# Kernel optimization log

Measured on AMD Instinct MI355X. Metric: run time of the kernel, lower is better.

The kernel has to match this reference:

```python
import jax, jax.numpy as jnp
import numpy as np

QUERY_DIM = 192
KEY_DIM = 64
DIM_OUT = 128
C = QUERY_DIM + KEY_DIM  # 256
N = 10000
E = 320000
M = 5000


def setup_inputs() -> dict:
    key = jax.random.key(0)
    ks = jax.random.split(key, 16)
    s = 1.0 / np.sqrt(C)
    inp = {
        "query": jax.random.normal(ks[0], (N, QUERY_DIM), jnp.float32),
        "key_idx": jax.random.randint(ks[1], (N,), 0, KEY_DIM),
        "edge_index": jax.random.randint(ks[2], (2, E), 0, N),
        "mask_idx": jnp.sort(jax.random.randint(ks[3], (M,), 0, N)),
        "Wq": jax.random.normal(ks[4], (C, C), jnp.float32) * s,
        "bq": jnp.zeros((C,), jnp.float32),
        "Wk": jax.random.normal(ks[5], (C, C), jnp.float32) * s,
        "bk": jnp.zeros((C,), jnp.float32),
        "Wv": jax.random.normal(ks[6], (C, C), jnp.float32) * s,
        "bv": jnp.zeros((C,), jnp.float32),
        "Ws": jax.random.normal(ks[7], (C, C), jnp.float32) * s,
        "bs": jnp.zeros((C,), jnp.float32),
        "Wo": jax.random.normal(ks[8], (KEY_DIM, DIM_OUT), jnp.float32) * (1.0 / np.sqrt(KEY_DIM)),
        "bo": jnp.zeros((DIM_OUT,), jnp.float32),
    }
    return inp


def reference(query, key_idx, edge_index, mask_idx, Wq, bq, Wk, bk, Wv, bv, Ws, bs, Wo, bo):
    # node features: [N, C] = concat(query, one_hot(key))
    x = jnp.concatenate([query, jax.nn.one_hot(key_idx, KEY_DIM, dtype=query.dtype)], axis=1)
    src, dst = edge_index[0], edge_index[1]  # messages flow src -> dst
    # node-level projections (dense GEMMs), then edge gather
    q_n = x @ Wq + bq
    k_n = x @ Wk + bk
    v_n = x @ Wv + bv
    q = q_n[dst]  # [E, C]
    k = k_n[src]
    v = v_n[src]
    score = jnp.sum(q * k, axis=-1) / jnp.sqrt(jnp.asarray(C, x.dtype))  # [E]
    # per-destination softmax over incoming edges
    m = jax.ops.segment_max(score, dst, num_segments=N)  # [N]
    m = jnp.where(jnp.isfinite(m), m, 0.0)
    e = jnp.exp(score - m[dst])
    denom = jax.ops.segment_sum(e, dst, num_segments=N)
    alpha = e / (denom[dst] + 1e-16)
    # scatter-aggregate weighted values + root/skip connection
    agg = jax.ops.segment_sum(alpha[:, None] * v, dst, num_segments=N)  # [N, C]
    out = agg + (x @ Ws + bs)
    h = jax.nn.relu(out[mask_idx])  # [M, C]
    h = h[:, QUERY_DIM:]  # [M, KEY_DIM]
    return h @ Wo + bo  # [M, DIM_OUT]
```

## Files before the change

### kernel.cpp

```cpp
#include <hip/hip_runtime.h>

#define QDIM 192
#define KDIM 64
#define CDIM 256
#define DOUT 128
#define CAP 128
#define NEG_INF __int_as_float(0xFF800000)
#define LDP 200

typedef _Float16 hf2 __attribute__((ext_vector_type(2)));
typedef _Float16 half4 __attribute__((ext_vector_type(4)));
typedef _Float16 half8 __attribute__((ext_vector_type(8)));
typedef float floatx4 __attribute__((ext_vector_type(4)));

#if defined(__has_builtin)
#if __has_builtin(__builtin_amdgcn_fdot2)
#define HAVE_FDOT2 1
#endif
#endif

__device__ __forceinline__ hf2 bc_h2(unsigned u) { return __builtin_bit_cast(hf2, u); }

__device__ __forceinline__ float dot2acc(hf2 a, hf2 b, float c) {
#ifdef HAVE_FDOT2
    return __builtin_amdgcn_fdot2(a, b, c, false);
#else
    return c + (float)a[0] * (float)b[0] + (float)a[1] * (float)b[1];
#endif
}

__global__ __launch_bounds__(256) void gemm_scatter(
        const float* __restrict__ query, const int* __restrict__ key_idx,
        const float* Wq, const float* bq, const float* Wk, const float* bk,
        const float* Wv, const float* bv, const float* Ws, const float* bs,
        const int* __restrict__ esrc, const int* __restrict__ edst,
        int* __restrict__ deg, int* __restrict__ adj, int E,
        _Float16* __restrict__ Qbuf, _Float16* __restrict__ Kbuf,
        _Float16* __restrict__ Vbuf, float* __restrict__ Sbuf, int N) {
    __shared__ __align__(16) _Float16 As[64 * LDP];
    __shared__ __align__(16) _Float16 Bs[64 * LDP];
    int bm = blockIdx.x * 64;
    int tid = threadIdx.x;

    {
        int total = gridDim.x * gridDim.y * 256;
        int gid = (blockIdx.y * gridDim.x + blockIdx.x) * 256 + tid;
        for (int e = gid; e < E; e += total) {
            int d = edst[e];
            int slot = atomicAdd(&deg[d], 1);
            if (slot < CAP) adj[d * CAP + slot] = esrc[e];
        }
    }

    #pragma unroll
    for (int it = 0; it < 12; it++) {
        int idx = tid + it * 256;
        int r = idx / 48, f4 = idx % 48;
        int gr = bm + r;
        float4 va = make_float4(0.f, 0.f, 0.f, 0.f);
        if (gr < N) va = ((const float4*)(query + (size_t)gr * QDIM))[f4];
        half4 h = { (_Float16)va.x, (_Float16)va.y, (_Float16)va.z, (_Float16)va.w };
        *((half4*)&As[r * LDP + f4 * 4]) = h;
    }

    int w = tid >> 6, l = tid & 63;
    int lrow = l & 15, quad = l >> 4;

    int ki[4];
    #pragma unroll
    for (int reg = 0; reg < 4; reg++) {
        int gr = bm + w * 16 + quad * 4 + reg;
        ki[reg] = (gr < N) ? key_idx[gr] : 0;
    }

    for (int t = 0; t < 2; t++) {
        int bn = blockIdx.y * 128 + t * 64;
        const float* Wb; const float* bvec; int wc0;
        if (bn < 256)      { Wb = Wq; bvec = bq; wc0 = bn; }
        else if (bn < 512) { Wb = Wk; bvec = bk; wc0 = bn - 256; }
        else if (bn < 576) { Wb = Wv; bvec = bv; wc0 = QDIM + (bn - 512); }
        else               { Wb = Ws; bvec = bs; wc0 = QDIM + (bn - 576); }

        if (t > 0) __syncthreads();
        {
            int c = tid & 63, r0 = tid >> 6;
            #pragma unroll
            for (int it = 0; it < 6; it++) {
                int kg = r0 + it * 4;
                float f[8];
                #pragma unroll
                for (int j = 0; j < 8; j++)
                    f[j] = Wb[(size_t)(kg * 8 + j) * CDIM + wc0 + c];
                half8 h8 = { (_Float16)f[0], (_Float16)f[1], (_Float16)f[2], (_Float16)f[3],
                             (_Float16)f[4], (_Float16)f[5], (_Float16)f[6], (_Float16)f[7] };
                *((half8*)&Bs[c * LDP + kg * 8]) = h8;
            }
        }
        __syncthreads();

        floatx4 acc[4] = {{0.f,0.f,0.f,0.f},{0.f,0.f,0.f,0.f},{0.f,0.f,0.f,0.f},{0.f,0.f,0.f,0.f}};
        const _Float16* arow = &As[(w * 16 + lrow) * LDP + quad * 8];
        #pragma unroll
        for (int ks = 0; ks < 6; ks++) {
            half8 af = *(const half8*)(arow + ks * 32);
            #pragma unroll
            for (int nt = 0; nt < 4; nt++) {
                half8 bf = *(const half8*)(&Bs[(nt * 16 + lrow) * LDP + quad * 8 + ks * 32]);
                acc[nt] = __builtin_amdgcn_mfma_f32_16x16x32_f16(af, bf, acc[nt], 0, 0, 0);
            }
        }

        #pragma unroll
        for (int nt = 0; nt < 4; nt++) {
            int gc = bn + nt * 16 + lrow;
            int wc = wc0 + nt * 16 + lrow;
            float bias = bvec[wc];
            #pragma unroll
            for (int reg = 0; reg < 4; reg++) {
                int gr = bm + w * 16 + quad * 4 + reg;
                if (gr < N) {
                    float v = acc[nt][reg] + Wb[(size_t)(QDIM + ki[reg]) * CDIM + wc] + bias;
                    if (gc < 256)      Qbuf[(size_t)gr * 256 + gc] = (_Float16)v;
                    else if (gc < 512) Kbuf[(size_t)gr * 256 + (gc - 256)] = (_Float16)v;
                    else if (gc < 576) Vbuf[(size_t)gr * KDIM + (gc - 512)] = (_Float16)v;
                    else               Sbuf[(size_t)gr * KDIM + (gc - 576)] = v;
                }
            }
        }
    }
}

__global__ __launch_bounds__(256) void attend_out(
        const _Float16* __restrict__ Qbuf, const _Float16* __restrict__ Kbuf,
        const _Float16* __restrict__ Vbuf, const float* __restrict__ Sbuf,
        const int* __restrict__ deg, const int* __restrict__ adj,
        const int* __restrict__ mask, const float* __restrict__ Wo,
        const float* __restrict__ bo, float* __restrict__ out, int M) {
    int w = threadIdx.x >> 6, lane = threadIdx.x & 63;
    int r = blockIdx.x * 4 + w;
    if (r >= M) return;
    int node = mask[r];
    if (r > 0 && mask[r - 1] == node) return;
    int l = lane & 15, g = lane >> 4;

    const uint4* qp = (const uint4*)(Qbuf + (size_t)node * 256 + l * 16);
    uint4 qa = qp[0], qb = qp[1];
    hf2 qh[8] = { bc_h2(qa.x), bc_h2(qa.y), bc_h2(qa.z), bc_h2(qa.w),
                  bc_h2(qb.x), bc_h2(qb.y), bc_h2(qb.z), bc_h2(qb.w) };

    int dn = min(deg[node], CAP);
    const int* arow = adj + (size_t)node * CAP;

    float m = NEG_INF, dsum = 0.f;
    float a0 = 0.f, a1 = 0.f, a2 = 0.f, a3 = 0.f;
    for (int i = g; i < dn; i += 4) {
        int s = arow[i];
        const uint4* kp = (const uint4*)(Kbuf + (size_t)s * 256 + l * 16);
        uint4 ka = kp[0], kb = kp[1];
        float d = 0.f;
        d = dot2acc(bc_h2(ka.x), qh[0], d);
        d = dot2acc(bc_h2(ka.y), qh[1], d);
        d = dot2acc(bc_h2(ka.z), qh[2], d);
        d = dot2acc(bc_h2(ka.w), qh[3], d);
        d = dot2acc(bc_h2(kb.x), qh[4], d);
        d = dot2acc(bc_h2(kb.y), qh[5], d);
        d = dot2acc(bc_h2(kb.z), qh[6], d);
        d = dot2acc(bc_h2(kb.w), qh[7], d);
        d += __shfl_xor(d, 1, 64);
        d += __shfl_xor(d, 2, 64);
        d += __shfl_xor(d, 4, 64);
        d += __shfl_xor(d, 8, 64);
        float sc = d * 0.0625f;
        float m_new = fmaxf(m, sc);
        float scale = __expf(m - m_new);
        float p = __expf(sc - m_new);
        dsum = dsum * scale + p;
        uint2 vv = *(const uint2*)(Vbuf + (size_t)s * KDIM + l * 4);
        hf2 v01 = bc_h2(vv.x), v23 = bc_h2(vv.y);
        a0 = a0 * scale + p * (float)v01[0];
        a1 = a1 * scale + p * (float)v01[1];
        a2 = a2 * scale + p * (float)v23[0];
        a3 = a3 * scale + p * (float)v23[1];
        m = m_new;
    }

    float Mx = fmaxf(m, __shfl_xor(m, 16, 64));
    Mx = fmaxf(Mx, __shfl_xor(Mx, 32, 64));
    float wgt = (m == NEG_INF) ? 0.f : __expf(m - Mx);
    float ds = dsum * wgt;
    ds += __shfl_xor(ds, 16, 64);
    ds += __shfl_xor(ds, 32, 64);
    a0 *= wgt; a1 *= wgt; a2 *= wgt; a3 *= wgt;
    a0 += __shfl_xor(a0, 16, 64); a0 += __shfl_xor(a0, 32, 64);
    a1 += __shfl_xor(a1, 16, 64); a1 += __shfl_xor(a1, 32, 64);
    a2 += __shfl_xor(a2, 16, 64); a2 += __shfl_xor(a2, 32, 64);
    a3 += __shfl_xor(a3, 16, 64); a3 += __shfl_xor(a3, 32, 64);
    float inv = 1.f / (ds + 1e-16f);

    float4 s4 = *((const float4*)(Sbuf + (size_t)node * KDIM + l * 4));
    float h0 = fmaxf(a0 * inv + s4.x, 0.f);
    float h1 = fmaxf(a1 * inv + s4.y, 0.f);
    float h2 = fmaxf(a2 * inv + s4.z, 0.f);
    float h3 = fmaxf(a3 * inv + s4.w, 0.f);

    float o0 = bo[lane], o1 = bo[lane + 64];
    #pragma unroll
    for (int c = 0; c < KDIM; c++) {
        float hc = (c & 3) == 0 ? h0 : (c & 3) == 1 ? h1 : (c & 3) == 2 ? h2 : h3;
        float hv = __shfl(hc, c >> 2, 64);
        o0 += hv * Wo[c * DOUT + lane];
        o1 += hv * Wo[c * DOUT + 64 + lane];
    }
    int rr = r;
    do {
        out[(size_t)rr * DOUT + lane] = o0;
        out[(size_t)rr * DOUT + 64 + lane] = o1;
        rr++;
    } while (rr < M && mask[rr] == node);
}

extern "C" void kernel_launch(void* const* d_in, const int* in_sizes, int n_in,
                              void* d_out, int out_size, void* d_ws, size_t ws_size,
                              hipStream_t stream) {
    const float* query    = (const float*)d_in[0];
    const int* key_idx    = (const int*)d_in[1];
    const int* edge_index = (const int*)d_in[2];
    const int* mask_idx   = (const int*)d_in[3];
    const float* Wq = (const float*)d_in[4];
    const float* bq = (const float*)d_in[5];
    const float* Wk = (const float*)d_in[6];
    const float* bk = (const float*)d_in[7];
    const float* Wv = (const float*)d_in[8];
    const float* bv = (const float*)d_in[9];
    const float* Ws = (const float*)d_in[10];
    const float* bs = (const float*)d_in[11];
    const float* Wo = (const float*)d_in[12];
    const float* bo = (const float*)d_in[13];

    int N = in_sizes[0] / QDIM;
    int E = in_sizes[2] / 2;
    int M = in_sizes[3];
    const int* esrc = edge_index;
    const int* edst = edge_index + E;

    char* wsb = (char*)d_ws;
    size_t off = 0;
    auto alloc = [&](size_t nbytes) { char* p = wsb + off; off += (nbytes + 15) & ~15ull; return p; };
    _Float16* Qbuf = (_Float16*)alloc((size_t)N * 256 * 2);
    _Float16* Kbuf = (_Float16*)alloc((size_t)N * 256 * 2);
    _Float16* Vbuf = (_Float16*)alloc((size_t)N * KDIM * 2);
    float* Sbuf    = (float*)alloc((size_t)N * KDIM * 4);
    int*   deg     = (int*)alloc((size_t)N * 4);
    int*   adj     = (int*)alloc((size_t)N * CAP * 4);

    hipMemsetAsync(deg, 0, (size_t)N * 4, stream);

    dim3 ggrid((N + 63) / 64, 5);
    gemm_scatter<<<ggrid, 256, 0, stream>>>(query, key_idx, Wq, bq, Wk, bk, Wv, bv,
                                            Ws, bs, esrc, edst, deg, adj, E,
                                            Qbuf, Kbuf, Vbuf, Sbuf, N);

    attend_out<<<(M + 3) / 4, 256, 0, stream>>>(Qbuf, Kbuf, Vbuf, Sbuf, deg, adj,
                                                mask_idx, Wo, bo, (float*)d_out, M);
}
```

Measured before the change: 151.6 us.

## Precast query and weights to fp16 in prep kernel, drop LDS staging in GEMM

Adds a prep kernel that converts the query to fp16 and writes a transposed fp16 copy of the needed weight columns, and also zeroes the degree array in place of the memset. The GEMM kernel then loads MFMA fragments straight from global memory into registers, with no shared-memory tiles and no barriers. This removes the per-block fp32-to-fp16 conversion and the strided, uncoalesced weight loads that were repeated in every block. In exchange it adds an extra kernel launch and an extra pass over the query, and B fragments are now read from global memory or cache rather than from LDS.

Result: slower. 157.8 us (+4.1%).

```diff
diff --git a/kernel.cpp b/kernel.cpp
--- a/kernel.cpp
+++ b/kernel.cpp
@@ -3,10 +3,10 @@
 #define QDIM 192
 #define KDIM 64
 #define CDIM 256
+#define NCOLS 640
 #define DOUT 128
 #define CAP 128
 #define NEG_INF __int_as_float(0xFF800000)
-#define LDP 200
 
 typedef _Float16 hf2 __attribute__((ext_vector_type(2)));
 typedef _Float16 half4 __attribute__((ext_vector_type(4)));
@@ -29,18 +29,50 @@
 #endif
 }
 
+__device__ __forceinline__ void wmap(int j, const float* Wq, const float* Wk,
+                                     const float* Wv, const float* Ws,
+                                     const float** W, int* wcol) {
+    if (j < 256)      { *W = Wq; *wcol = j; }
+    else if (j < 512) { *W = Wk; *wcol = j - 256; }
+    else if (j < 576) { *W = Wv; *wcol = QDIM + (j - 512); }
+    else              { *W = Ws; *wcol = QDIM + (j - 576); }
+}
+
+__global__ __launch_bounds__(256) void prep_kernel(
+        const float* __restrict__ query,
+        const float* Wq, const float* Wk, const float* Wv, const float* Ws,
+        _Float16* __restrict__ Qh, _Float16* __restrict__ BhT,
+        int* __restrict__ deg, int qchunks, int N) {
+    int t = blockIdx.x * blockDim.x + threadIdx.x;
+    if (t < qchunks) {
+        float4 v = ((const float4*)query)[t];
+        half4 h = { (_Float16)v.x, (_Float16)v.y, (_Float16)v.z, (_Float16)v.w };
+        ((half4*)Qh)[t] = h;
+        return;
+    }
+    t -= qchunks;
+    if (t < NCOLS * QDIM) {
+        int n = t / QDIM, k = t % QDIM;
+        const float* W; int wc;
+        wmap(n, Wq, Wk, Wv, Ws, &W, &wc);
+        BhT[t] = (_Float16)W[k * CDIM + wc];
+        return;
+    }
+    t -= NCOLS * QDIM;
+    if (t < N) deg[t] = 0;
+}
+
 __global__ __launch_bounds__(256) void gemm_scatter(
-        const float* __restrict__ query, const int* __restrict__ key_idx,
+        const _Float16* __restrict__ Qh, const _Float16* __restrict__ BhT,
+        const int* __restrict__ key_idx,
         const float* Wq, const float* bq, const float* Wk, const float* bk,
         const float* Wv, const float* bv, const float* Ws, const float* bs,
         const int* __restrict__ esrc, const int* __restrict__ edst,
         int* __restrict__ deg, int* __restrict__ adj, int E,
         _Float16* __restrict__ Qbuf, _Float16* __restrict__ Kbuf,
         _Float16* __restrict__ Vbuf, float* __restrict__ Sbuf, int N) {
-    __shared__ __align__(16) _Float16 As[64 * LDP];
-    __shared__ __align__(16) _Float16 Bs[64 * LDP];
+    int tid = threadIdx.x;
     int bm = blockIdx.x * 64;
-    int tid = threadIdx.x;
 
     {
         int total = gridDim.x * gridDim.y * 256;
@@ -52,19 +84,21 @@
         }
     }
 
-    #pragma unroll
-    for (int it = 0; it < 12; it++) {
-        int idx = tid + it * 256;
-        int r = idx / 48, f4 = idx % 48;
-        int gr = bm + r;
-        float4 va = make_float4(0.f, 0.f, 0.f, 0.f);
-        if (gr < N) va = ((const float4*)(query + (size_t)gr * QDIM))[f4];
-        half4 h = { (_Float16)va.x, (_Float16)va.y, (_Float16)va.z, (_Float16)va.w };
-        *((half4*)&As[r * LDP + f4 * 4]) = h;
-    }
-
     int w = tid >> 6, l = tid & 63;
     int lrow = l & 15, quad = l >> 4;
+
+    int gr_a = bm + w * 16 + lrow;
+    half8 af[6];
+    {
+        const _Float16* ap = Qh + (size_t)gr_a * QDIM + quad * 8;
+        bool ok = (gr_a < N);
+        #pragma unroll
+        for (int ks = 0; ks < 6; ks++) {
+            half8 z = { (_Float16)0.f, (_Float16)0.f, (_Float16)0.f, (_Float16)0.f,
+                        (_Float16)0.f, (_Float16)0.f, (_Float16)0.f, (_Float16)0.f };
+            af[ks] = ok ? *(const half8*)(ap + ks * 32) : z;
+        }
+    }
 
     int ki[4];
     #pragma unroll
@@ -73,6 +107,7 @@
         ki[reg] = (gr < N) ? key_idx[gr] : 0;
     }
 
+    #pragma unroll
     for (int t = 0; t < 2; t++) {
         int bn = blockIdx.y * 128 + t * 64;
         const float* Wb; const float* bvec; int wc0;
@@ -81,32 +116,14 @@
         else if (bn < 576) { Wb = Wv; bvec = bv; wc0 = QDIM + (bn - 512); }
         else               { Wb = Ws; bvec = bs; wc0 = QDIM + (bn - 576); }
 
-        if (t > 0) __syncthreads();
-        {
-            int c = tid & 63, r0 = tid >> 6;
-            #pragma unroll
-            for (int it = 0; it < 6; it++) {
-                int kg = r0 + it * 4;
-                float f[8];
-                #pragma unroll
-                for (int j = 0; j < 8; j++)
-                    f[j] = Wb[(size_t)(kg * 8 + j) * CDIM + wc0 + c];
-                half8 h8 = { (_Float16)f[0], (_Float16)f[1], (_Float16)f[2], (_Float16)f[3],
-                             (_Float16)f[4], (_Float16)f[5], (_Float16)f[6], (_Float16)f[7] };
-                *((half8*)&Bs[c * LDP + kg * 8]) = h8;
-            }
-        }
-        __syncthreads();
-
         floatx4 acc[4] = {{0.f,0.f,0.f,0.f},{0.f,0.f,0.f,0.f},{0.f,0.f,0.f,0.f},{0.f,0.f,0.f,0.f}};
-        const _Float16* arow = &As[(w * 16 + lrow) * LDP + quad * 8];
+        const _Float16* bp = BhT + (size_t)(bn + lrow) * QDIM + quad * 8;
         #pragma unroll
         for (int ks = 0; ks < 6; ks++) {
-            half8 af = *(const half8*)(arow + ks * 32);
             #pragma unroll
             for (int nt = 0; nt < 4; nt++) {
-                half8 bf = *(const half8*)(&Bs[(nt * 16 + lrow) * LDP + quad * 8 + ks * 32]);
-                acc[nt] = __builtin_amdgcn_mfma_f32_16x16x32_f16(af, bf, acc[nt], 0, 0, 0);
+                half8 bf = *(const half8*)(bp + (size_t)nt * 16 * QDIM + ks * 32);
+                acc[nt] = __builtin_amdgcn_mfma_f32_16x16x32_f16(af[ks], bf, acc[nt], 0, 0, 0);
             }
         }
 
@@ -246,6 +263,8 @@
     char* wsb = (char*)d_ws;
     size_t off = 0;
     auto alloc = [&](size_t nbytes) { char* p = wsb + off; off += (nbytes + 15) & ~15ull; return p; };
+    _Float16* Qh   = (_Float16*)alloc((size_t)N * QDIM * 2);
+    _Float16* BhT  = (_Float16*)alloc((size_t)NCOLS * QDIM * 2);
     _Float16* Qbuf = (_Float16*)alloc((size_t)N * 256 * 2);
     _Float16* Kbuf = (_Float16*)alloc((size_t)N * 256 * 2);
     _Float16* Vbuf = (_Float16*)alloc((size_t)N * KDIM * 2);
@@ -253,10 +272,13 @@
     int*   deg     = (int*)alloc((size_t)N * 4);
     int*   adj     = (int*)alloc((size_t)N * CAP * 4);
 
-    hipMemsetAsync(deg, 0, (size_t)N * 4, stream);
+    int qchunks = N * QDIM / 4;
+    int prep_elems = qchunks + NCOLS * QDIM + N;
+    prep_kernel<<<(prep_elems + 255) / 256, 256, 0, stream>>>(
+        query, Wq, Wk, Wv, Ws, Qh, BhT, deg, qchunks, N);
 
     dim3 ggrid((N + 63) / 64, 5);
-    gemm_scatter<<<ggrid, 256, 0, stream>>>(query, key_idx, Wq, bq, Wk, bk, Wv, bv,
+    gemm_scatter<<<ggrid, 256, 0, stream>>>(Qh, BhT, key_idx, Wq, bq, Wk, bk, Wv, bv,
                                             Ws, bs, esrc, edst, deg, adj, E,
                                             Qbuf, Kbuf, Vbuf, Sbuf, N);
 
```
